# Performance work log

Hardware: AMD Instinct MI355X
Metric: run time of the kernel (lower is better)

Reference implementation:

```python
import jax, jax.numpy as jnp
import numpy as np

T = 3
R = 0.05  # threshold on SQUARED distance (as in the source: dis < r)
N, M = 4, 384

_PSPEC = [("hW1", (3, 64)), ("hb1", (64,)), ("hW2", (64, 128)), ("hb2", (128,)), ("hW3", (128, 3)), ("hb3", (3,)),
          ("fW1", (6, 64)), ("fb1", (64,)), ("fW2", (64, 128)), ("fb2", (128,)), ("fW3", (128, 128)), ("fb3", (128,)),
          ("gW1", (128, 64)), ("gb1", (64,)), ("gW2", (64, 32)), ("gb2", (32,)), ("gW3", (32, 3)), ("gb3", (3,))]


def setup_inputs() -> dict:
    key = jax.random.key(0)
    inp = {"x": jax.random.uniform(key, (N, M, 3), jnp.float32)}
    for i, (name, shp) in enumerate(_PSPEC):
        k = jax.random.fold_in(key, i + 1)
        scale = 1.0 / np.sqrt(shp[0]) if len(shp) == 2 else 0.01
        inp[name] = jax.random.normal(k, (T,) + shp, jnp.float32) * jnp.float32(scale)
    return inp


def _mlp(x, W1, b1, W2, b2, W3, b3, final_relu):
    h = jax.nn.relu(x @ W1 + b1)
    h = jax.nn.relu(h @ W2 + b2)
    o = h @ W3 + b3
    return jax.nn.relu(o) if final_relu else o


def _forward(x, hW1, hb1, hW2, hb2, hW3, hb3, fW1, fb1, fW2, fb2, fW3, fb3, gW1, gb1, gW2, gb2, gW3, gb3):
    n, m, _ = x.shape
    diff = x[:, :, None, :] - x[:, None, :, :]              # (N,M,M,3)
    adj = jnp.sum(diff * diff, axis=-1) < R                 # (N,M,M) squared-dist ball
    state = x
    for t in range(T):
        # NOTE on MLP_h / delta: in the source, xj and xi inside getTimeEdges are
        # IDENTICAL broadcasts of xi_delta (both x.unsqueeze(-2).repeat over dim -2),
        # so xi[adj] = xj[adj] - xi[adj] == 0 everywhere. The relative-position
        # slot is therefore exactly zeros and delta = MLP_h(state) never affects
        # the output (and receives zero gradient in torch as well).
        rel = jnp.zeros((n, m, m, 3), x.dtype)
        # state[n,i,j,:] = state[n,j,:] where adj[n,i,j], else 0
        sfull = jnp.where(adj[..., None], state[:, None, :, :], 0.0)  # (N,M,M,3)
        eij = jnp.concatenate([rel, sfull], axis=-1)                   # (N,M,M,6)
        e = _mlp(eij, fW1[t], fb1[t], fW2[t], fb2[t], fW3[t], fb3[t], True)  # (N,M,M,128)
        e = jnp.where(adj[..., None], e, 0.0)
        agg = jnp.max(e, axis=2)                                       # max over neighbors j -> (N,M,128)
        state = _mlp(agg, gW1[t], gb1[t], gW2[t], gb2[t], gW3[t], gb3[t], True) + state
    return state


def reference(x, hW1, hb1, hW2, hb2, hW3, hb3, fW1, fb1, fW2, fb2, fW3, fb3, gW1, gb1, gW2, gb2, gW3, gb3):
    return _forward(x, hW1, hb1, hW2, hb2, hW3, hb3, fW1, fb1, fW2, fb2, fW3, fb3, gW1, gb1, gW2, gb2, gW3, gb3)
```

## Files before the change

### kernel.cpp

```cpp
#include <hip/hip_runtime.h>

#define MNODES 384
#define RTHRESH 0.05f


__global__ __launch_bounds__(256) void adj_kernel(const float* __restrict__ x,
                                                  int* __restrict__ cnt,
                                                  unsigned short* __restrict__ lists) {
    __shared__ float xs[MNODES * 3];
    const int tid = threadIdx.x;
    const int wv = tid >> 6, lane = tid & 63;
    const int node = blockIdx.x * 4 + wv;
    const int n = blockIdx.x / 96;
    const int i = node - n * MNODES;

    for (int idx = tid; idx < MNODES * 3; idx += 256)
        xs[idx] = x[n * MNODES * 3 + idx];
    __syncthreads();

    const float xi0 = xs[i * 3], xi1 = xs[i * 3 + 1], xi2 = xs[i * 3 + 2];
    unsigned short* ml = lists + (size_t)node * MNODES;
    int total = 0;
#pragma unroll
    for (int rep = 0; rep < 6; ++rep) {
        const int j = rep * 64 + lane;
        float dx = xs[j * 3] - xi0;
        float dy = xs[j * 3 + 1] - xi1;
        float dz = xs[j * 3 + 2] - xi2;
        float d2 = __fadd_rn(__fadd_rn(__fmul_rn(dx, dx), __fmul_rn(dy, dy)), __fmul_rn(dz, dz));
        const bool a = d2 < RTHRESH;
        const unsigned long long m = __ballot(a);
        if (a) {
            const int pos = total + __popcll(m & ((1ull << lane) - 1ull));
            ml[pos] = (unsigned short)j;
        }
        total += (int)__popcll(m);
    }
    if (lane == 0) cnt[node] = total;
}

__global__ __launch_bounds__(256) void phi_kernel(const float* __restrict__ state,
                                                  const float* __restrict__ fW1,
                                                  const float* __restrict__ fb1,
                                                  const float* __restrict__ fW2,
                                                  const float* __restrict__ fb2,
                                                  const float* __restrict__ fW3,
                                                  const float* __restrict__ fb3,
                                                  float* __restrict__ phi) {
    __shared__ float H1[4][64];
    __shared__ float H2[4][128];
    const int tid = threadIdx.x;
    const int wv = tid >> 6, lane = tid & 63;
    const int node = blockIdx.x * 4 + wv;

    float sv = 0.0f;
    if (lane < 3) sv = state[node * 3 + lane];
    const float s0 = __shfl(sv, 0), s1 = __shfl(sv, 1), s2 = __shfl(sv, 2);

    float v = fb1[lane];
    v = fmaf(s0, fW1[3 * 64 + lane], v);
    v = fmaf(s1, fW1[4 * 64 + lane], v);
    v = fmaf(s2, fW1[5 * 64 + lane], v);
    H1[wv][lane] = fmaxf(v, 0.0f);
    __syncthreads();

    float a0 = fb2[lane], a1 = fb2[lane + 64];
#pragma unroll 8
    for (int c = 0; c < 64; ++c) {
        const float h = H1[wv][c];
        a0 = fmaf(h, fW2[c * 128 + lane], a0);
        a1 = fmaf(h, fW2[c * 128 + lane + 64], a1);
    }
    H2[wv][lane] = fmaxf(a0, 0.0f);
    H2[wv][lane + 64] = fmaxf(a1, 0.0f);
    __syncthreads();

    float c0 = fb3[lane], c1 = fb3[lane + 64];
#pragma unroll 8
    for (int c = 0; c < 128; ++c) {
        const float h = H2[wv][c];
        c0 = fmaf(h, fW3[c * 128 + lane], c0);
        c1 = fmaf(h, fW3[c * 128 + lane + 64], c1);
    }
    phi[(size_t)node * 128 + lane] = fmaxf(c0, 0.0f);
    phi[(size_t)node * 128 + lane + 64] = fmaxf(c1, 0.0f);
}

__global__ __launch_bounds__(256) void aggg_kernel(const float* __restrict__ phi,
                                                   const int* __restrict__ cnt,
                                                   const unsigned short* __restrict__ lists,
                                                   const float* __restrict__ statesrc,
                                                   const float* __restrict__ gW1,
                                                   const float* __restrict__ gb1,
                                                   const float* __restrict__ gW2,
                                                   const float* __restrict__ gb2,
                                                   const float* __restrict__ gW3,
                                                   const float* __restrict__ gb3,
                                                   float* __restrict__ dst) {
    __shared__ float aggL[4][128];
    __shared__ float h1L[4][64];
    __shared__ float h2L[4][32];
    const int tid = threadIdx.x;
    const int wv = tid >> 6, lane = tid & 63;
    const int node = __builtin_amdgcn_readfirstlane(blockIdx.x * 4 + wv);
    const int nbase = (blockIdx.x / 96) * MNODES;
    const int nc = cnt[node];
    const unsigned short* ml = lists + (size_t)node * MNODES;
    const float* pb = phi + (size_t)nbase * 128;

    float m0 = 0.f, m1 = 0.f, m2 = 0.f, m3 = 0.f;
    float p0 = 0.f, p1 = 0.f, p2 = 0.f, p3 = 0.f;
    int jj = 0;
    for (; jj + 4 <= nc; jj += 4) {
        const int j0 = ml[jj], j1 = ml[jj + 1], j2 = ml[jj + 2], j3 = ml[jj + 3];
        const float* r0 = pb + (size_t)j0 * 128;
        const float* r1 = pb + (size_t)j1 * 128;
        const float* r2 = pb + (size_t)j2 * 128;
        const float* r3 = pb + (size_t)j3 * 128;
        m0 = fmaxf(m0, r0[lane]); p0 = fmaxf(p0, r0[lane + 64]);
        m1 = fmaxf(m1, r1[lane]); p1 = fmaxf(p1, r1[lane + 64]);
        m2 = fmaxf(m2, r2[lane]); p2 = fmaxf(p2, r2[lane + 64]);
        m3 = fmaxf(m3, r3[lane]); p3 = fmaxf(p3, r3[lane + 64]);
    }
    for (; jj < nc; ++jj) {
        const int j = ml[jj];
        const float* r = pb + (size_t)j * 128;
        m0 = fmaxf(m0, r[lane]); p0 = fmaxf(p0, r[lane + 64]);
    }
    aggL[wv][lane] = fmaxf(fmaxf(m0, m1), fmaxf(m2, m3));
    aggL[wv][lane + 64] = fmaxf(fmaxf(p0, p1), fmaxf(p2, p3));
    __syncthreads();

    float h = gb1[lane];
#pragma unroll 8
    for (int c = 0; c < 128; ++c) h = fmaf(aggL[wv][c], gW1[c * 64 + lane], h);
    h1L[wv][lane] = fmaxf(h, 0.0f);
    __syncthreads();

    if (lane < 32) {
        float v = gb2[lane];
#pragma unroll 8
        for (int k = 0; k < 64; ++k) v = fmaf(h1L[wv][k], gW2[k * 32 + lane], v);
        h2L[wv][lane] = fmaxf(v, 0.0f);
    }
    __syncthreads();

    if (lane < 3) {
        float o = gb3[lane];
#pragma unroll
        for (int m = 0; m < 32; ++m) o = fmaf(h2L[wv][m], gW3[m * 3 + lane], o);
        dst[node * 3 + lane] = fmaxf(o, 0.0f) + statesrc[node * 3 + lane];
    }
}

extern "C" void kernel_launch(void* const* d_in, const int* in_sizes, int n_in,
                              void* d_out, int out_size, void* d_ws, size_t ws_size,
                              hipStream_t stream) {
    const float* x   = (const float*)d_in[0];
    const float* fW1 = (const float*)d_in[7];
    const float* fb1 = (const float*)d_in[8];
    const float* fW2 = (const float*)d_in[9];
    const float* fb2 = (const float*)d_in[10];
    const float* fW3 = (const float*)d_in[11];
    const float* fb3 = (const float*)d_in[12];
    const float* gW1 = (const float*)d_in[13];
    const float* gb1 = (const float*)d_in[14];
    const float* gW2 = (const float*)d_in[15];
    const float* gb2 = (const float*)d_in[16];
    const float* gW3 = (const float*)d_in[17];
    const float* gb3 = (const float*)d_in[18];

    char* ws = (char*)d_ws;
    float* state          = (float*)(ws + 0);
    int* cnt              = (int*)(ws + 18432);
    unsigned short* lists = (unsigned short*)(ws + 24576);
    float* phi            = (float*)(ws + 1204224);

    adj_kernel<<<384, 256, 0, stream>>>(x, cnt, lists);

    for (int t = 0; t < 3; ++t) {
        const float* src = (t == 0) ? x : state;
        float* dst = (t == 2) ? (float*)d_out : state;
        phi_kernel<<<384, 256, 0, stream>>>(src,
                                            fW1 + t * 6 * 64, fb1 + t * 64,
                                            fW2 + t * 64 * 128, fb2 + t * 128,
                                            fW3 + t * 128 * 128, fb3 + t * 128,
                                            phi);
        aggg_kernel<<<384, 256, 0, stream>>>(phi, cnt, lists, src,
                                             gW1 + t * 128 * 64, gb1 + t * 64,
                                             gW2 + t * 64 * 32, gb2 + t * 32,
                                             gW3 + t * 32 * 3, gb3 + t * 3,
                                             dst);
    }
}
```

Baseline: 154.5 us.

## Fuse all stages into one cooperative persistent kernel with grid syncs

```diff
diff --git a/kernel.cpp b/kernel.cpp
--- a/kernel.cpp
+++ b/kernel.cpp
@@ -1,118 +1,59 @@
 #include <hip/hip_runtime.h>
+#include <hip/hip_cooperative_groups.h>
+
+namespace cg = cooperative_groups;
 
 #define MNODES 384
 #define RTHRESH 0.05f
 
 
-__global__ __launch_bounds__(256) void adj_kernel(const float* __restrict__ x,
-                                                  int* __restrict__ cnt,
-                                                  unsigned short* __restrict__ lists) {
-    __shared__ float xs[MNODES * 3];
-    const int tid = threadIdx.x;
-    const int wv = tid >> 6, lane = tid & 63;
-    const int node = blockIdx.x * 4 + wv;
-    const int n = blockIdx.x / 96;
-    const int i = node - n * MNODES;
-
-    for (int idx = tid; idx < MNODES * 3; idx += 256)
-        xs[idx] = x[n * MNODES * 3 + idx];
-    __syncthreads();
-
-    const float xi0 = xs[i * 3], xi1 = xs[i * 3 + 1], xi2 = xs[i * 3 + 2];
-    unsigned short* ml = lists + (size_t)node * MNODES;
-    int total = 0;
-#pragma unroll
-    for (int rep = 0; rep < 6; ++rep) {
-        const int j = rep * 64 + lane;
-        float dx = xs[j * 3] - xi0;
-        float dy = xs[j * 3 + 1] - xi1;
-        float dz = xs[j * 3 + 2] - xi2;
-        float d2 = __fadd_rn(__fadd_rn(__fmul_rn(dx, dx), __fmul_rn(dy, dy)), __fmul_rn(dz, dz));
-        const bool a = d2 < RTHRESH;
-        const unsigned long long m = __ballot(a);
-        if (a) {
-            const int pos = total + __popcll(m & ((1ull << lane) - 1ull));
-            ml[pos] = (unsigned short)j;
-        }
-        total += (int)__popcll(m);
-    }
-    if (lane == 0) cnt[node] = total;
-}
-
-__global__ __launch_bounds__(256) void phi_kernel(const float* __restrict__ state,
-                                                  const float* __restrict__ fW1,
-                                                  const float* __restrict__ fb1,
-                                                  const float* __restrict__ fW2,
-                                                  const float* __restrict__ fb2,
-                                                  const float* __restrict__ fW3,
-                                                  const float* __restrict__ fb3,
-                                                  float* __restrict__ phi) {
-    __shared__ float H1[4][64];
-    __shared__ float H2[4][128];
-    const int tid = threadIdx.x;
-    const int wv = tid >> 6, lane = tid & 63;
-    const int node = blockIdx.x * 4 + wv;
-
-    float sv = 0.0f;
-    if (lane < 3) sv = state[node * 3 + lane];
-    const float s0 = __shfl(sv, 0), s1 = __shfl(sv, 1), s2 = __shfl(sv, 2);
-
+__device__ __forceinline__ void phi_stage(
+    const float* __restrict__ fW1, const float* __restrict__ fb1,
+    const float* __restrict__ fW2, const float* __restrict__ fb2,
+    const float* __restrict__ fW3, const float* __restrict__ fb3,
+    float s0, float s1, float s2, int lane,
+    float* __restrict__ H1, float* __restrict__ H2,
+    float* __restrict__ phidst )
+{
     float v = fb1[lane];
     v = fmaf(s0, fW1[3 * 64 + lane], v);
     v = fmaf(s1, fW1[4 * 64 + lane], v);
     v = fmaf(s2, fW1[5 * 64 + lane], v);
-    H1[wv][lane] = fmaxf(v, 0.0f);
-    __syncthreads();
-
+    H1[lane] = fmaxf(v, 0.0f);
     float a0 = fb2[lane], a1 = fb2[lane + 64];
 #pragma unroll 8
     for (int c = 0; c < 64; ++c) {
-        const float h = H1[wv][c];
+        const float h = H1[c];
         a0 = fmaf(h, fW2[c * 128 + lane], a0);
         a1 = fmaf(h, fW2[c * 128 + lane + 64], a1);
     }
-    H2[wv][lane] = fmaxf(a0, 0.0f);
-    H2[wv][lane + 64] = fmaxf(a1, 0.0f);
-    __syncthreads();
-
+    H2[lane] = fmaxf(a0, 0.0f);
+    H2[lane + 64] = fmaxf(a1, 0.0f);
     float c0 = fb3[lane], c1 = fb3[lane + 64];
 #pragma unroll 8
     for (int c = 0; c < 128; ++c) {
-        const float h = H2[wv][c];
+        const float h = H2[c];
         c0 = fmaf(h, fW3[c * 128 + lane], c0);
         c1 = fmaf(h, fW3[c * 128 + lane + 64], c1);
     }
-    phi[(size_t)node * 128 + lane] = fmaxf(c0, 0.0f);
-    phi[(size_t)node * 128 + lane + 64] = fmaxf(c1, 0.0f);
-}
-
-__global__ __launch_bounds__(256) void aggg_kernel(const float* __restrict__ phi,
-                                                   const int* __restrict__ cnt,
-                                                   const unsigned short* __restrict__ lists,
-                                                   const float* __restrict__ statesrc,
-                                                   const float* __restrict__ gW1,
-                                                   const float* __restrict__ gb1,
-                                                   const float* __restrict__ gW2,
-                                                   const float* __restrict__ gb2,
-                                                   const float* __restrict__ gW3,
-                                                   const float* __restrict__ gb3,
-                                                   float* __restrict__ dst) {
-    __shared__ float aggL[4][128];
-    __shared__ float h1L[4][64];
-    __shared__ float h2L[4][32];
-    const int tid = threadIdx.x;
-    const int wv = tid >> 6, lane = tid & 63;
-    const int node = __builtin_amdgcn_readfirstlane(blockIdx.x * 4 + wv);
-    const int nbase = (blockIdx.x / 96) * MNODES;
-    const int nc = cnt[node];
-    const unsigned short* ml = lists + (size_t)node * MNODES;
-    const float* pb = phi + (size_t)nbase * 128;
-
+    phidst[lane] = fmaxf(c0, 0.0f);
+    phidst[lane + 64] = fmaxf(c1, 0.0f);
+}
+
+__device__ __forceinline__ float aggg_stage(
+    const float* __restrict__ pb ,
+    const unsigned short* __restrict__ nl, int nc,
+    const float* __restrict__ gW1, const float* __restrict__ gb1,
+    const float* __restrict__ gW2, const float* __restrict__ gb2,
+    const float* __restrict__ gW3, const float* __restrict__ gb3,
+    int lane, float* __restrict__ aggL, float* __restrict__ h1L,
+    float* __restrict__ h2L)
+{
     float m0 = 0.f, m1 = 0.f, m2 = 0.f, m3 = 0.f;
     float p0 = 0.f, p1 = 0.f, p2 = 0.f, p3 = 0.f;
     int jj = 0;
     for (; jj + 4 <= nc; jj += 4) {
-        const int j0 = ml[jj], j1 = ml[jj + 1], j2 = ml[jj + 2], j3 = ml[jj + 3];
+        const int j0 = nl[jj], j1 = nl[jj + 1], j2 = nl[jj + 2], j3 = nl[jj + 3];
         const float* r0 = pb + (size_t)j0 * 128;
         const float* r1 = pb + (size_t)j1 * 128;
         const float* r2 = pb + (size_t)j2 * 128;
@@ -123,33 +64,107 @@
         m3 = fmaxf(m3, r3[lane]); p3 = fmaxf(p3, r3[lane + 64]);
     }
     for (; jj < nc; ++jj) {
-        const int j = ml[jj];
+        const int j = nl[jj];
         const float* r = pb + (size_t)j * 128;
         m0 = fmaxf(m0, r[lane]); p0 = fmaxf(p0, r[lane + 64]);
     }
-    aggL[wv][lane] = fmaxf(fmaxf(m0, m1), fmaxf(m2, m3));
-    aggL[wv][lane + 64] = fmaxf(fmaxf(p0, p1), fmaxf(p2, p3));
+    aggL[lane] = fmaxf(fmaxf(m0, m1), fmaxf(m2, m3));
+    aggL[lane + 64] = fmaxf(fmaxf(p0, p1), fmaxf(p2, p3));
+    float h = gb1[lane];
+#pragma unroll 8
+    for (int c = 0; c < 128; ++c) h = fmaf(aggL[c], gW1[c * 64 + lane], h);
+    h1L[lane] = fmaxf(h, 0.0f);
+    if (lane < 32) {
+        float v2 = gb2[lane];
+#pragma unroll 8
+        for (int k = 0; k < 64; ++k) v2 = fmaf(h1L[k], gW2[k * 32 + lane], v2);
+        h2L[lane] = fmaxf(v2, 0.0f);
+    }
+    float o = 0.0f;
+    if (lane < 3) {
+        float v3 = gb3[lane];
+#pragma unroll
+        for (int m = 0; m < 32; ++m) v3 = fmaf(h2L[m], gW3[m * 3 + lane], v3);
+        o = fmaxf(v3, 0.0f);
+    }
+    return o;
+}
+
+__global__ __launch_bounds__(384) void fused_gnn(
+    const float* __restrict__ x,
+    const float* __restrict__ fW1, const float* __restrict__ fb1,
+    const float* __restrict__ fW2, const float* __restrict__ fb2,
+    const float* __restrict__ fW3, const float* __restrict__ fb3,
+    const float* __restrict__ gW1, const float* __restrict__ gb1,
+    const float* __restrict__ gW2, const float* __restrict__ gb2,
+    const float* __restrict__ gW3, const float* __restrict__ gb3,
+    float* __restrict__ phiA, float* __restrict__ phiB,
+    float* __restrict__ out)
+{
+    cg::grid_group grid = cg::this_grid();
+
+    __shared__ float xs[MNODES * 3];
+    __shared__ float work[6][224];
+    __shared__ unsigned short nlist[6][384];
+
+    const int tid = threadIdx.x;
+    const int wv = tid >> 6, lane = tid & 63;
+    const int blk = blockIdx.x;
+    const int node = blk * 6 + wv;
+    const int n = blk >> 6;
+    const int i = node - n * MNODES;
+    const int nbase = n * MNODES;
+
+    for (int idx = tid; idx < MNODES * 3; idx += 384)
+        xs[idx] = x[n * MNODES * 3 + idx];
     __syncthreads();
 
-    float h = gb1[lane];
-#pragma unroll 8
-    for (int c = 0; c < 128; ++c) h = fmaf(aggL[wv][c], gW1[c * 64 + lane], h);
-    h1L[wv][lane] = fmaxf(h, 0.0f);
-    __syncthreads();
-
-    if (lane < 32) {
-        float v = gb2[lane];
-#pragma unroll 8
-        for (int k = 0; k < 64; ++k) v = fmaf(h1L[wv][k], gW2[k * 32 + lane], v);
-        h2L[wv][lane] = fmaxf(v, 0.0f);
-    }
-    __syncthreads();
-
-    if (lane < 3) {
-        float o = gb3[lane];
+    float s0 = xs[i * 3 + 0], s1 = xs[i * 3 + 1], s2 = xs[i * 3 + 2];
+
+    int nc = 0;
+    {
+        unsigned short* ml = &nlist[wv][0];
 #pragma unroll
-        for (int m = 0; m < 32; ++m) o = fmaf(h2L[wv][m], gW3[m * 3 + lane], o);
-        dst[node * 3 + lane] = fmaxf(o, 0.0f) + statesrc[node * 3 + lane];
+        for (int rep = 0; rep < 6; ++rep) {
+            const int j = rep * 64 + lane;
+            float dx = xs[j * 3 + 0] - s0;
+            float dy = xs[j * 3 + 1] - s1;
+            float dz = xs[j * 3 + 2] - s2;
+            float d2 = __fadd_rn(__fadd_rn(__fmul_rn(dx, dx), __fmul_rn(dy, dy)),
+                                 __fmul_rn(dz, dz));
+            const bool a = d2 < RTHRESH;
+            const unsigned long long m = __ballot(a);
+            if (a) ml[nc + __popcll(m & ((1ull << lane) - 1ull))] = (unsigned short)j;
+            nc += (int)__popcll(m);
+        }
+    }
+
+    float* const H1 = &work[wv][0];
+    float* const H2 = &work[wv][64];
+    phi_stage(fW1, fb1, fW2, fb2, fW3, fb3, s0, s1, s2, lane, H1, H2,
+              phiA + (size_t)node * 128);
+    grid.sync();
+
+    for (int t = 0; t < 3; ++t) {
+        const float* psrc = (t & 1) ? phiB : phiA;
+        const float o = aggg_stage(psrc + (size_t)nbase * 128, &nlist[wv][0], nc,
+                                   gW1 + t * 8192, gb1 + t * 64,
+                                   gW2 + t * 2048, gb2 + t * 32,
+                                   gW3 + t * 96, gb3 + t * 3,
+                                   lane, &work[wv][0], &work[wv][128], &work[wv][192]);
+        const float ns = o + ((lane == 0) ? s0 : (lane == 1) ? s1 : s2);
+        s0 = __shfl(ns, 0); s1 = __shfl(ns, 1); s2 = __shfl(ns, 2);
+        if (t == 2) {
+            if (lane < 3) out[node * 3 + lane] = ns;
+        } else {
+            const int tn = t + 1;
+            float* pdst = (tn & 1) ? phiB : phiA;
+            phi_stage(fW1 + tn * 384, fb1 + tn * 64,
+                      fW2 + tn * 8192, fb2 + tn * 128,
+                      fW3 + tn * 16384, fb3 + tn * 128,
+                      s0, s1, s2, lane, H1, H2, pdst + (size_t)node * 128);
+            grid.sync();
+        }
     }
 }
 
@@ -170,26 +185,16 @@
     const float* gW3 = (const float*)d_in[17];
     const float* gb3 = (const float*)d_in[18];
 
-    char* ws = (char*)d_ws;
-    float* state          = (float*)(ws + 0);
-    int* cnt              = (int*)(ws + 18432);
-    unsigned short* lists = (unsigned short*)(ws + 24576);
-    float* phi            = (float*)(ws + 1204224);
-
-    adj_kernel<<<384, 256, 0, stream>>>(x, cnt, lists);
-
-    for (int t = 0; t < 3; ++t) {
-        const float* src = (t == 0) ? x : state;
-        float* dst = (t == 2) ? (float*)d_out : state;
-        phi_kernel<<<384, 256, 0, stream>>>(src,
-                                            fW1 + t * 6 * 64, fb1 + t * 64,
-                                            fW2 + t * 64 * 128, fb2 + t * 128,
-                                            fW3 + t * 128 * 128, fb3 + t * 128,
-                                            phi);
-        aggg_kernel<<<384, 256, 0, stream>>>(phi, cnt, lists, src,
-                                             gW1 + t * 128 * 64, gb1 + t * 64,
-                                             gW2 + t * 64 * 32, gb2 + t * 32,
-                                             gW3 + t * 32 * 3, gb3 + t * 3,
-                                             dst);
-    }
-}
+    float* phiA = (float*)d_ws;
+    float* phiB = (float*)((char*)d_ws + 786432);
+    float* outp = (float*)d_out;
+
+    void* args[] = {
+        (void*)&x,
+        (void*)&fW1, (void*)&fb1, (void*)&fW2, (void*)&fb2, (void*)&fW3, (void*)&fb3,
+        (void*)&gW1, (void*)&gb1, (void*)&gW2, (void*)&gb2, (void*)&gW3, (void*)&gb3,
+        (void*)&phiA, (void*)&phiB, (void*)&outp
+    };
+    hipLaunchCooperativeKernel((const void*)fused_gnn, dim3(256), dim3(384),
+                               args, 0, stream);
+}
```

Result: slower. 246.2 us (+59.4%).
